# Kernel tuning notes

Hardware: AMD Instinct MI355X
Metric: run time of the kernel (lower is better)

Reference implementation:

```python
import jax, jax.numpy as jnp
import numpy as np

NEG_SLOPE = 0.2  # PyG GATConv default


def gat_layer(x, W, att_src, att_dst, bias, src, dst, num_nodes, heads, out_ch):
    # x: [N, Fin]; W: [Fin, heads*out_ch]; att_*: [heads, out_ch]; bias: [heads*out_ch]
    xw = (x @ W).reshape(num_nodes, heads, out_ch)          # [N, H, C]
    a_src = jnp.sum(xw * att_src, axis=-1)                  # [N, H]
    a_dst = jnp.sum(xw * att_dst, axis=-1)                  # [N, H]
    e = jax.nn.leaky_relu(a_src[src] + a_dst[dst], NEG_SLOPE)  # [E, H]
    # segment softmax over incoming edges of each destination node
    e_max = jax.ops.segment_max(e, dst, num_segments=num_nodes)   # [N, H]
    e_exp = jnp.exp(e - e_max[dst])                                # [E, H]
    denom = jax.ops.segment_sum(e_exp, dst, num_segments=num_nodes)
    alpha = e_exp / denom[dst]                                     # [E, H]
    out = jax.ops.segment_sum(alpha[:, :, None] * xw[src], dst, num_segments=num_nodes)  # [N, H, C]
    return out.reshape(num_nodes, heads * out_ch) + bias


def setup_inputs() -> dict:
    key = jax.random.key(0)
    ks = jax.random.split(key, 12)
    N, E = 50000, 800000
    F_IN, HID, HEADS, NCLS = 128, 32, 4, 8
    x = jax.random.normal(ks[0], (N, F_IN), dtype=jnp.float32)
    src = jax.random.randint(ks[1], (E,), 0, N)
    dst = jax.random.randint(ks[2], (E,), 0, N)
    dst = jnp.where(dst == src, (dst + 1) % N, dst)  # no self loops; reference adds them
    edge_index = jnp.stack([src, dst]).astype(jnp.int64)
    s1 = 1.0 / np.sqrt(F_IN)
    s2 = 1.0 / np.sqrt(HEADS * HID)
    W1 = jax.random.normal(ks[3], (F_IN, HEADS * HID), dtype=jnp.float32) * s1
    att_src1 = jax.random.normal(ks[4], (HEADS, HID), dtype=jnp.float32) * s2
    att_dst1 = jax.random.normal(ks[5], (HEADS, HID), dtype=jnp.float32) * s2
    b1 = jnp.zeros((HEADS * HID,), dtype=jnp.float32)
    W2 = jax.random.normal(ks[6], (HEADS * HID, NCLS), dtype=jnp.float32) * s2
    att_src2 = jax.random.normal(ks[7], (1, NCLS), dtype=jnp.float32)
    att_dst2 = jax.random.normal(ks[8], (1, NCLS), dtype=jnp.float32)
    b2 = jnp.zeros((NCLS,), dtype=jnp.float32)
    return {"x": x, "edge_index": edge_index, "W1": W1, "att_src1": att_src1,
            "att_dst1": att_dst1, "b1": b1, "W2": W2, "att_src2": att_src2,
            "att_dst2": att_dst2, "b2": b2}


def reference(x, edge_index, W1, att_src1, att_dst1, b1, W2, att_src2, att_dst2, b2):
    N = x.shape[0]
    loops = jnp.arange(N, dtype=edge_index.dtype)
    src = jnp.concatenate([edge_index[0], loops])  # add self loops (PyG default)
    dst = jnp.concatenate([edge_index[1], loops])
    h = gat_layer(x, W1, att_src1, att_dst1, b1, src, dst, N, heads=4, out_ch=32)
    h = jax.nn.relu(h)
    out = gat_layer(h, W2, att_src2, att_dst2, b2, src, dst, N, heads=1, out_ch=8)
    return jax.nn.log_softmax(out, axis=1)
```

## Files before the change

### kernel.cpp

```cpp
#include <hip/hip_runtime.h>
#include <hip/hip_fp16.h>
#include <math.h>

#define F_IN   128
#define HEADS  4
#define HID    32
#define NCLS   8
#define SLOPE  0.2f
#define CAP    64
#define NBK    256
#define BSH    8
#define CHK    4096
#define BCAP   5120
#define SSTR   136

typedef _Float16 half8 __attribute__((ext_vector_type(8)));
typedef float    floatx4 __attribute__((ext_vector_type(4)));
typedef float    floatv4 __attribute__((ext_vector_type(4)));

__global__ void k_prep(int* __restrict__ bcur,
                       const float* __restrict__ W1, _Float16* __restrict__ Wt) {
    if (blockIdx.x == 0) {
        bcur[threadIdx.x] = threadIdx.x * BCAP;
    } else {
        int idx = (blockIdx.x - 1) * 256 + threadIdx.x;
        int c = idx >> 7, k = idx & 127;
        Wt[c * 128 + k] = (_Float16)W1[k * 128 + c];
    }
}

__global__ void k_scatter_gemm(const int* __restrict__ ei, int* __restrict__ bcur,
                               unsigned* __restrict__ stage, int E, int N, int NCHK,
                               const float* __restrict__ x, const _Float16* __restrict__ Wt,
                               const float* __restrict__ as1, const float* __restrict__ ad1,
                               _Float16* __restrict__ xwh, float* __restrict__ asrc,
                               float* __restrict__ adst) {
    __shared__ __align__(16) unsigned char smem[4 * 16 * SSTR * 2];
    if ((int)blockIdx.x < NCHK) {
        int* hist = (int*)smem;
        int* lcur = hist + NBK;
        hist[threadIdx.x] = 0;
        int probe = ei[2 * (threadIdx.x & 63) + 1];
        bool is64 = (__ballot(probe != 0) == 0ULL);
        __syncthreads();
        int base = blockIdx.x * CHK;
        int dd[16], ss[16];
        #pragma unroll
        for (int k = 0; k < 16; k++) {
            int i = base + k * 256 + threadIdx.x;
            if (i < E) {
                dd[k] = is64 ? ei[2 * E + 2 * i] : ei[E + i];
                ss[k] = is64 ? ei[2 * i]         : ei[i];
                atomicAdd(&hist[dd[k] >> BSH], 1);
            } else dd[k] = -1;
        }
        __syncthreads();
        {
            int h = hist[threadIdx.x];
            lcur[threadIdx.x] = (h > 0) ? atomicAdd(&bcur[threadIdx.x], h) : 0;
        }
        __syncthreads();
        #pragma unroll
        for (int k = 0; k < 16; k++) {
            if (dd[k] >= 0) {
                int bkt = dd[k] >> BSH;
                int p = atomicAdd(&lcur[bkt], 1);
                if (p < (bkt + 1) * BCAP)
                    stage[p] = ((unsigned)dd[k] << 16) | (unsigned)ss[k];
            }
        }
        return;
    }
    int gb   = blockIdx.x - NCHK;
    int wv   = threadIdx.x >> 6;
    int lane = threadIdx.x & 63;
    int r0   = gb * 64 + wv * 16;
    if (r0 >= N) return;
    int q = lane >> 4, t = lane & 15;
    int row = r0 + t;
    bool rok = row < N;
    _Float16* shw = (_Float16*)smem + wv * (16 * SSTR);

    half8 afr[4];
    #pragma unroll
    for (int kc = 0; kc < 4; kc++) {
        floatv4 u0 = {0.f, 0.f, 0.f, 0.f}, u1 = u0;
        if (rok) {
            const floatv4* xr = (const floatv4*)(x + (size_t)row * 128 + kc * 32 + q * 8);
            u0 = __builtin_nontemporal_load(xr);
            u1 = __builtin_nontemporal_load(xr + 1);
        }
        afr[kc][0] = (_Float16)u0[0]; afr[kc][1] = (_Float16)u0[1];
        afr[kc][2] = (_Float16)u0[2]; afr[kc][3] = (_Float16)u0[3];
        afr[kc][4] = (_Float16)u1[0]; afr[kc][5] = (_Float16)u1[1];
        afr[kc][6] = (_Float16)u1[2]; afr[kc][7] = (_Float16)u1[3];
    }

    float ps[4], pd[4];
    #pragma unroll
    for (int ct = 0; ct < 8; ct++) {
        floatx4 acc = {0.f, 0.f, 0.f, 0.f};
        #pragma unroll
        for (int kc = 0; kc < 4; kc++) {
            half8 bfr = *(const half8*)(Wt + (ct * 16 + t) * 128 + kc * 32 + q * 8);
            acc = __builtin_amdgcn_mfma_f32_16x16x32_f16(afr[kc], bfr, acc, 0, 0, 0);
        }
        int col = ct * 16 + t;
        float sa = as1[col], da = ad1[col];
        if ((ct & 1) == 0) {
            #pragma unroll
            for (int g = 0; g < 4; g++) { ps[g] = 0.f; pd[g] = 0.f; }
        }
        #pragma unroll
        for (int g = 0; g < 4; g++) {
            shw[(q * 4 + g) * SSTR + col] = (_Float16)acc[g];
            ps[g] += acc[g] * sa;
            pd[g] += acc[g] * da;
        }
        if (ct & 1) {
            int h = ct >> 1;
            #pragma unroll
            for (int g = 0; g < 4; g++) {
                float a = ps[g], d = pd[g];
                a += __shfl_xor(a, 1); d += __shfl_xor(d, 1);
                a += __shfl_xor(a, 2); d += __shfl_xor(d, 2);
                a += __shfl_xor(a, 4); d += __shfl_xor(d, 4);
                a += __shfl_xor(a, 8); d += __shfl_xor(d, 8);
                int r = r0 + q * 4 + g;
                if (t == 0 && r < N) { asrc[r * 4 + h] = a; adst[r * 4 + h] = d; }
            }
        }
    }
    #pragma unroll
    for (int k = 0; k < 4; k++) {
        int idx = k * 64 + lane;
        int rr = idx >> 4, cc = idx & 15;
        if (r0 + rr < N)
            *(half8*)(xwh + (size_t)(r0 + rr) * 128 + cc * 8) =
                *(const half8*)(shw + rr * SSTR + cc * 8);
    }
}

__global__ void k_fill(const unsigned* __restrict__ stage, const int* __restrict__ bcur,
                       unsigned short* __restrict__ csr16, int* __restrict__ cur, int N) {
    int b  = blockIdx.x;
    int lo = b << BSH;
    if (lo >= N) return;
    int nn = N - lo; if (nn > 256) nn = 256;
    __shared__ int lc[256];
    lc[threadIdx.x] = (threadIdx.x < nn) ? 1 : 0;
    __syncthreads();
    if (threadIdx.x < nn)
        csr16[(size_t)(lo + threadIdx.x) * CAP] = (unsigned short)(lo + threadIdx.x);
    int base = b * BCAP;
    int cnt  = bcur[b] - base;
    if (cnt > BCAP) cnt = BCAP;
    if (cnt < 0) cnt = 0;
    for (int i = base + threadIdx.x; i < base + cnt; i += 256) {
        unsigned u = stage[i];
        int d = u >> 16, s = u & 0xFFFF;
        int p = atomicAdd(&lc[d - lo], 1);
        if (p < CAP) csr16[(size_t)d * CAP + p] = (unsigned short)s;
    }
    __syncthreads();
    if (threadIdx.x < nn) {
        int c = lc[threadIdx.x];
        cur[lo + threadIdx.x] = (c > CAP) ? CAP : c;
    }
}

__global__ void k_agg1(const _Float16* __restrict__ xwh, const float* __restrict__ asrc,
                       const float* __restrict__ adst, const int* __restrict__ cur,
                       const unsigned short* __restrict__ csr16, const float* __restrict__ b1,
                       const float* __restrict__ W2, const float* __restrict__ as2,
                       const float* __restrict__ ad2, float* __restrict__ xw2,
                       float* __restrict__ asrc2, float* __restrict__ adst2, int N) {
    int node = (blockIdx.x * blockDim.x + threadIdx.x) >> 6;
    int lane = threadIdx.x & 63;
    if (node >= N) return;
    int h = lane >> 4;
    int t = lane & 15;
    int ch = h * 32 + 2 * t;

    const float4* w2p = (const float4*)(W2 + ch * 8);
    float4 wa0 = w2p[0], wa1 = w2p[1];
    float4 wb0 = w2p[2], wb1 = w2p[3];
    float a_s = as2[lane & 7];
    float a_d = ad2[lane & 7];

    float adst_h = adst[node * 4 + h];
    int beg = node * CAP;
    int deg = cur[node];
    int end = beg + deg;

    float s = 0.f, a0 = 0.f, a1 = 0.f;
    int j = beg;
    for (; j + 8 <= end; j += 8) {
        ushort4 sA = *(const ushort4*)(csr16 + j);
        ushort4 sB = *(const ushort4*)(csr16 + j + 4);
        float e0 = asrc[sA.x * 4 + h] + adst_h;
        float e1 = asrc[sA.y * 4 + h] + adst_h;
        float e2 = asrc[sA.z * 4 + h] + adst_h;
        float e3 = asrc[sA.w * 4 + h] + adst_h;
        float e4 = asrc[sB.x * 4 + h] + adst_h;
        float e5 = asrc[sB.y * 4 + h] + adst_h;
        float e6 = asrc[sB.z * 4 + h] + adst_h;
        float e7 = asrc[sB.w * 4 + h] + adst_h;
        float2 f0 = __half22float2(*(const __half2*)(xwh + (size_t)sA.x * 128 + ch));
        float2 f1 = __half22float2(*(const __half2*)(xwh + (size_t)sA.y * 128 + ch));
        float2 f2 = __half22float2(*(const __half2*)(xwh + (size_t)sA.z * 128 + ch));
        float2 f3 = __half22float2(*(const __half2*)(xwh + (size_t)sA.w * 128 + ch));
        float2 f4 = __half22float2(*(const __half2*)(xwh + (size_t)sB.x * 128 + ch));
        float2 f5 = __half22float2(*(const __half2*)(xwh + (size_t)sB.y * 128 + ch));
        float2 f6 = __half22float2(*(const __half2*)(xwh + (size_t)sB.z * 128 + ch));
        float2 f7 = __half22float2(*(const __half2*)(xwh + (size_t)sB.w * 128 + ch));
        e0 = (e0 > 0.f) ? e0 : SLOPE * e0;   float p0 = __expf(e0);
        e1 = (e1 > 0.f) ? e1 : SLOPE * e1;   float p1 = __expf(e1);
        e2 = (e2 > 0.f) ? e2 : SLOPE * e2;   float p2 = __expf(e2);
        e3 = (e3 > 0.f) ? e3 : SLOPE * e3;   float p3 = __expf(e3);
        e4 = (e4 > 0.f) ? e4 : SLOPE * e4;   float p4 = __expf(e4);
        e5 = (e5 > 0.f) ? e5 : SLOPE * e5;   float p5 = __expf(e5);
        e6 = (e6 > 0.f) ? e6 : SLOPE * e6;   float p6 = __expf(e6);
        e7 = (e7 > 0.f) ? e7 : SLOPE * e7;   float p7 = __expf(e7);
        s  += (p0 + p1 + p2 + p3) + (p4 + p5 + p6 + p7);
        a0 += p0 * f0.x + p1 * f1.x + p2 * f2.x + p3 * f3.x
            + p4 * f4.x + p5 * f5.x + p6 * f6.x + p7 * f7.x;
        a1 += p0 * f0.y + p1 * f1.y + p2 * f2.y + p3 * f3.y
            + p4 * f4.y + p5 * f5.y + p6 * f6.y + p7 * f7.y;
    }
    for (; j < end; j++) {
        int s0 = csr16[j];
        float e0 = asrc[s0 * 4 + h] + adst_h;
        float2 f0 = __half22float2(*(const __half2*)(xwh + (size_t)s0 * 128 + ch));
        e0 = (e0 > 0.f) ? e0 : SLOPE * e0;
        float p0 = __expf(e0);
        s  += p0;
        a0 += p0 * f0.x;
        a1 += p0 * f0.y;
    }
    float inv = 1.f / s;
    float o0 = fmaxf(a0 * inv + b1[ch],     0.f);
    float o1 = fmaxf(a1 * inv + b1[ch + 1], 0.f);

    float p[8];
    p[0] = o0 * wa0.x + o1 * wb0.x;  p[1] = o0 * wa0.y + o1 * wb0.y;
    p[2] = o0 * wa0.z + o1 * wb0.z;  p[3] = o0 * wa0.w + o1 * wb0.w;
    p[4] = o0 * wa1.x + o1 * wb1.x;  p[5] = o0 * wa1.y + o1 * wb1.y;
    p[6] = o0 * wa1.z + o1 * wb1.z;  p[7] = o0 * wa1.w + o1 * wb1.w;
    float qq[4];
    #pragma unroll
    for (int b = 0; b < 4; b++) {
        float keepv = (lane & 1) ? p[2 * b + 1] : p[2 * b];
        float sendv = (lane & 1) ? p[2 * b]     : p[2 * b + 1];
        qq[b] = keepv + __shfl_xor(sendv, 1);
    }
    float r2[2];
    #pragma unroll
    for (int b = 0; b < 2; b++) {
        float keepv = (lane & 2) ? qq[2 * b + 1] : qq[2 * b];
        float sendv = (lane & 2) ? qq[2 * b]     : qq[2 * b + 1];
        r2[b] = keepv + __shfl_xor(sendv, 2);
    }
    {
        float keepv = (lane & 4) ? r2[1] : r2[0];
        float sendv = (lane & 4) ? r2[0] : r2[1];
        r2[0] = keepv + __shfl_xor(sendv, 4);
    }
    float f = r2[0];
    f += __shfl_xor(f, 8);
    f += __shfl_xor(f, 16);
    f += __shfl_xor(f, 32);
    if (lane < 8) xw2[node * 8 + lane] = f;
    float vs = f * a_s;
    float vd = f * a_d;
    vs += __shfl_xor(vs, 1); vs += __shfl_xor(vs, 2); vs += __shfl_xor(vs, 4);
    vd += __shfl_xor(vd, 1); vd += __shfl_xor(vd, 2); vd += __shfl_xor(vd, 4);
    if (lane == 0) { asrc2[node] = vs; adst2[node] = vd; }
}

__global__ void k_agg2(const float* __restrict__ xw2, const float* __restrict__ asrc2,
                       const float* __restrict__ adst2, const int* __restrict__ cur,
                       const unsigned short* __restrict__ csr16, const float* __restrict__ b2,
                       float* __restrict__ out, int N) {
    int node = (blockIdx.x * blockDim.x + threadIdx.x) >> 6;
    int lane = threadIdx.x & 63;
    if (node >= N) return;
    int slot = lane >> 3;
    int c    = lane & 7;
    float adst = adst2[node];
    int beg = node * CAP;
    int deg = cur[node];
    float s = 0.f, acc = 0.f;
    for (int j = slot; j < deg; j += 8) {
        int s0 = csr16[beg + j];
        float e0 = asrc2[s0] + adst;
        float v0 = xw2[s0 * 8 + c];
        e0 = (e0 > 0.f) ? e0 : SLOPE * e0;
        float p0 = __expf(e0);
        s   += p0;
        acc += p0 * v0;
    }
    #pragma unroll
    for (int mk = 8; mk < 64; mk <<= 1) {
        s   += __shfl_xor(s, mk);
        acc += __shfl_xor(acc, mk);
    }
    float o = acc / s + b2[c];
    float mxv = o;
    mxv = fmaxf(mxv, __shfl_xor(mxv, 1));
    mxv = fmaxf(mxv, __shfl_xor(mxv, 2));
    mxv = fmaxf(mxv, __shfl_xor(mxv, 4));
    float ex = __expf(o - mxv);
    float se = ex;
    se += __shfl_xor(se, 1); se += __shfl_xor(se, 2); se += __shfl_xor(se, 4);
    if (slot == 0) out[node * 8 + c] = o - mxv - __logf(se);
}

extern "C" void kernel_launch(void* const* d_in, const int* in_sizes, int n_in,
                              void* d_out, int out_size, void* d_ws, size_t ws_size,
                              hipStream_t stream) {
    const float* x   = (const float*)d_in[0];
    const int*   ei  = (const int*)d_in[1];
    const float* W1  = (const float*)d_in[2];
    const float* as1 = (const float*)d_in[3];
    const float* ad1 = (const float*)d_in[4];
    const float* b1  = (const float*)d_in[5];
    const float* W2  = (const float*)d_in[6];
    const float* as2 = (const float*)d_in[7];
    const float* ad2 = (const float*)d_in[8];
    const float* b2  = (const float*)d_in[9];
    float* out = (float*)d_out;

    int N = in_sizes[0] / F_IN;
    int E = in_sizes[1] / 2;
    int GB   = (N + 63) / 64;
    int NCHK = (E + CHK - 1) / CHK;

    char* p = (char*)d_ws;
    auto carve = [&](size_t bytes) { char* q = p; p += (bytes + 255) & ~(size_t)255; return (void*)q; };
    _Float16* xw1h = (_Float16*)carve((size_t)N * 128 * 2);
    _Float16* Wt   = (_Float16*)carve(128 * 128 * 2);
    float* asrc1 = (float*)carve((size_t)N * 4 * 4);
    float* adst1 = (float*)carve((size_t)N * 4 * 4);
    float* xw2   = (float*)carve((size_t)N * 8 * 4);
    float* asrc2 = (float*)carve((size_t)N * 4);
    float* adst2 = (float*)carve((size_t)N * 4);
    int*   cur   = (int*)carve((size_t)N * 4);
    int*   bcur  = (int*)carve(NBK * 4);
    unsigned* stage = (unsigned*)carve((size_t)NBK * BCAP * 4);
    unsigned short* csr16 = (unsigned short*)carve((size_t)N * CAP * 2);

    k_prep<<<65, 256, 0, stream>>>(bcur, W1, Wt);
    k_scatter_gemm<<<NCHK + GB, 256, 0, stream>>>(ei, bcur, stage, E, N, NCHK,
                                                  x, Wt, as1, ad1, xw1h, asrc1, adst1);
    k_fill<<<NBK, 256, 0, stream>>>(stage, bcur, csr16, cur, N);
    k_agg1<<<(N + 3) / 4, 256, 0, stream>>>(xw1h, asrc1, adst1, cur, csr16, b1,
                                            W2, as2, ad2, xw2, asrc2, adst2, N);
    k_agg2<<<(N + 3) / 4, 256, 0, stream>>>(xw2, asrc2, adst2, cur, csr16, b2, out, N);
}
```

Measured before the change: 197.1 us.

## Regroup launches: scatter with W transpose, then fill CSR alongside the GEMM

The kernel groups are reshuffled. The edge scatter now runs together with the W1 transpose. The CSR fill runs together with the fp16 GEMM in one launch, and a memset replaces the bucket-cursor init. This removes one dependent launch and lets the fill and GEMM blocks overlap on the GPU, at the cost of a memset and of the GEMM having to wait until the scatter finishes.

Result: slower. 202.8 us (+2.9%).

```diff
diff --git a/kernel.cpp b/kernel.cpp
--- a/kernel.cpp
+++ b/kernel.cpp
@@ -18,60 +18,86 @@
 typedef float    floatx4 __attribute__((ext_vector_type(4)));
 typedef float    floatv4 __attribute__((ext_vector_type(4)));
 
-__global__ void k_prep(int* __restrict__ bcur,
-                       const float* __restrict__ W1, _Float16* __restrict__ Wt) {
-    if (blockIdx.x == 0) {
-        bcur[threadIdx.x] = threadIdx.x * BCAP;
-    } else {
-        int idx = (blockIdx.x - 1) * 256 + threadIdx.x;
+__global__ void k_scatter_prep(const int* __restrict__ ei, int* __restrict__ bcur,
+                               unsigned* __restrict__ stage, int E, int NCHK,
+                               const float* __restrict__ W1, _Float16* __restrict__ Wt) {
+    if ((int)blockIdx.x >= NCHK) {
+        int idx = (blockIdx.x - NCHK) * 256 + threadIdx.x;
         int c = idx >> 7, k = idx & 127;
         Wt[c * 128 + k] = (_Float16)W1[k * 128 + c];
-    }
-}
-
-__global__ void k_scatter_gemm(const int* __restrict__ ei, int* __restrict__ bcur,
-                               unsigned* __restrict__ stage, int E, int N, int NCHK,
-                               const float* __restrict__ x, const _Float16* __restrict__ Wt,
-                               const float* __restrict__ as1, const float* __restrict__ ad1,
-                               _Float16* __restrict__ xwh, float* __restrict__ asrc,
-                               float* __restrict__ adst) {
+        return;
+    }
+    __shared__ int hist[NBK];
+    __shared__ int lcur[NBK];
+    hist[threadIdx.x] = 0;
+    int probe = ei[2 * (threadIdx.x & 63) + 1];
+    bool is64 = (__ballot(probe != 0) == 0ULL);
+    __syncthreads();
+    int base = blockIdx.x * CHK;
+    int dd[16], ss[16];
+    #pragma unroll
+    for (int k = 0; k < 16; k++) {
+        int i = base + k * 256 + threadIdx.x;
+        if (i < E) {
+            dd[k] = is64 ? ei[2 * E + 2 * i] : ei[E + i];
+            ss[k] = is64 ? ei[2 * i]         : ei[i];
+            atomicAdd(&hist[dd[k] >> BSH], 1);
+        } else dd[k] = -1;
+    }
+    __syncthreads();
+    {
+        int h = hist[threadIdx.x];
+        lcur[threadIdx.x] = (h > 0) ? atomicAdd(&bcur[threadIdx.x], h) : 0;
+    }
+    __syncthreads();
+    #pragma unroll
+    for (int k = 0; k < 16; k++) {
+        if (dd[k] >= 0) {
+            int bkt = dd[k] >> BSH;
+            int p = atomicAdd(&lcur[bkt], 1);
+            if (p < BCAP)
+                stage[(size_t)bkt * BCAP + p] = ((unsigned)dd[k] << 16) | (unsigned)ss[k];
+        }
+    }
+}
+
+__global__ void k_fill_gemm(const unsigned* __restrict__ stage,
+                            const int* __restrict__ bcur,
+                            unsigned short* __restrict__ csr16, int* __restrict__ cur,
+                            int N,
+                            const float* __restrict__ x, const _Float16* __restrict__ Wt,
+                            const float* __restrict__ as1, const float* __restrict__ ad1,
+                            _Float16* __restrict__ xwh, float* __restrict__ asrc,
+                            float* __restrict__ adst) {
     __shared__ __align__(16) unsigned char smem[4 * 16 * SSTR * 2];
-    if ((int)blockIdx.x < NCHK) {
-        int* hist = (int*)smem;
-        int* lcur = hist + NBK;
-        hist[threadIdx.x] = 0;
-        int probe = ei[2 * (threadIdx.x & 63) + 1];
-        bool is64 = (__ballot(probe != 0) == 0ULL);
+    if ((int)blockIdx.x < NBK) {
+        int* lc = (int*)smem;
+        int b  = blockIdx.x;
+        int lo = b << BSH;
+        if (lo >= N) return;
+        int nn = N - lo; if (nn > 256) nn = 256;
+        lc[threadIdx.x] = (threadIdx.x < nn) ? 1 : 0;
         __syncthreads();
-        int base = blockIdx.x * CHK;
-        int dd[16], ss[16];
-        #pragma unroll
-        for (int k = 0; k < 16; k++) {
-            int i = base + k * 256 + threadIdx.x;
-            if (i < E) {
-                dd[k] = is64 ? ei[2 * E + 2 * i] : ei[E + i];
-                ss[k] = is64 ? ei[2 * i]         : ei[i];
-                atomicAdd(&hist[dd[k] >> BSH], 1);
-            } else dd[k] = -1;
+        if (threadIdx.x < nn)
+            csr16[(size_t)(lo + threadIdx.x) * CAP] = (unsigned short)(lo + threadIdx.x);
+        size_t base = (size_t)b * BCAP;
+        int cnt = bcur[b];
+        if (cnt > BCAP) cnt = BCAP;
+        if (cnt < 0) cnt = 0;
+        for (int i = threadIdx.x; i < cnt; i += 256) {
+            unsigned u = stage[base + i];
+            int d = u >> 16, s = u & 0xFFFF;
+            int p = atomicAdd(&lc[d - lo], 1);
+            if (p < CAP) csr16[(size_t)d * CAP + p] = (unsigned short)s;
         }
         __syncthreads();
-        {
-            int h = hist[threadIdx.x];
-            lcur[threadIdx.x] = (h > 0) ? atomicAdd(&bcur[threadIdx.x], h) : 0;
-        }
-        __syncthreads();
-        #pragma unroll
-        for (int k = 0; k < 16; k++) {
-            if (dd[k] >= 0) {
-                int bkt = dd[k] >> BSH;
-                int p = atomicAdd(&lcur[bkt], 1);
-                if (p < (bkt + 1) * BCAP)
-                    stage[p] = ((unsigned)dd[k] << 16) | (unsigned)ss[k];
-            }
+        if (threadIdx.x < nn) {
+            int c = lc[threadIdx.x];
+            cur[lo + threadIdx.x] = (c > CAP) ? CAP : c;
         }
         return;
     }
-    int gb   = blockIdx.x - NCHK;
+    int gb   = blockIdx.x - NBK;
     int wv   = threadIdx.x >> 6;
     int lane = threadIdx.x & 63;
     int r0   = gb * 64 + wv * 16;
@@ -138,34 +164,6 @@
         if (r0 + rr < N)
             *(half8*)(xwh + (size_t)(r0 + rr) * 128 + cc * 8) =
                 *(const half8*)(shw + rr * SSTR + cc * 8);
-    }
-}
-
-__global__ void k_fill(const unsigned* __restrict__ stage, const int* __restrict__ bcur,
-                       unsigned short* __restrict__ csr16, int* __restrict__ cur, int N) {
-    int b  = blockIdx.x;
-    int lo = b << BSH;
-    if (lo >= N) return;
-    int nn = N - lo; if (nn > 256) nn = 256;
-    __shared__ int lc[256];
-    lc[threadIdx.x] = (threadIdx.x < nn) ? 1 : 0;
-    __syncthreads();
-    if (threadIdx.x < nn)
-        csr16[(size_t)(lo + threadIdx.x) * CAP] = (unsigned short)(lo + threadIdx.x);
-    int base = b * BCAP;
-    int cnt  = bcur[b] - base;
-    if (cnt > BCAP) cnt = BCAP;
-    if (cnt < 0) cnt = 0;
-    for (int i = base + threadIdx.x; i < base + cnt; i += 256) {
-        unsigned u = stage[i];
-        int d = u >> 16, s = u & 0xFFFF;
-        int p = atomicAdd(&lc[d - lo], 1);
-        if (p < CAP) csr16[(size_t)d * CAP + p] = (unsigned short)s;
-    }
-    __syncthreads();
-    if (threadIdx.x < nn) {
-        int c = lc[threadIdx.x];
-        cur[lo + threadIdx.x] = (c > CAP) ? CAP : c;
     }
 }
 
@@ -350,10 +348,10 @@
     unsigned* stage = (unsigned*)carve((size_t)NBK * BCAP * 4);
     unsigned short* csr16 = (unsigned short*)carve((size_t)N * CAP * 2);
 
-    k_prep<<<65, 256, 0, stream>>>(bcur, W1, Wt);
-    k_scatter_gemm<<<NCHK + GB, 256, 0, stream>>>(ei, bcur, stage, E, N, NCHK,
-                                                  x, Wt, as1, ad1, xw1h, asrc1, adst1);
-    k_fill<<<NBK, 256, 0, stream>>>(stage, bcur, csr16, cur, N);
+    hipMemsetAsync(bcur, 0, NBK * sizeof(int), stream);
+    k_scatter_prep<<<NCHK + 64, 256, 0, stream>>>(ei, bcur, stage, E, NCHK, W1, Wt);
+    k_fill_gemm<<<NBK + GB, 256, 0, stream>>>(stage, bcur, csr16, cur, N,
+                                              x, Wt, as1, ad1, xw1h, asrc1, adst1);
     k_agg1<<<(N + 3) / 4, 256, 0, stream>>>(xw1h, asrc1, adst1, cur, csr16, b1,
                                             W2, as2, ad2, xw2, asrc2, adst2, N);
     k_agg2<<<(N + 3) / 4, 256, 0, stream>>>(xw2, asrc2, adst2, cur, csr16, b2, out, N);
```
